# Performance work log

Measured on AMD Instinct MI355X. Metric: run time of the kernel, lower is better.

Reference implementation:

```python
import jax, jax.numpy as jnp
import numpy as np
import math

B, T, C = 4, 2048, 1024
N_HEADS = 16
D_HEAD = C // N_HEADS


def _rope_tables(d_head, max_seq_len):
    half = d_head // 2
    theta = 1.0 / (10000.0 ** (jnp.arange(half, dtype=jnp.float32) / half))
    pos = jnp.arange(max_seq_len, dtype=jnp.float32)
    freqs = jnp.outer(pos, theta)  # [S, half]
    cos = jnp.concatenate([jnp.cos(freqs), jnp.cos(freqs)], axis=-1)  # [S, d_head]
    sin = jnp.concatenate([jnp.sin(freqs), jnp.sin(freqs)], axis=-1)
    return cos, sin


def _rotate_half(x):
    d = x.shape[-1] // 2
    return jnp.concatenate([-x[..., d:], x[..., :d]], axis=-1)


def _apply_rope(x, cos, sin):
    # x: [B, H, T, d_head]; cos/sin: [T, d_head] broadcast over B,H
    return x * cos[None, None] + _rotate_half(x) * sin[None, None]


def setup_inputs() -> dict:
    key = jax.random.key(0)
    k1, k2, k3 = jax.random.split(key, 3)
    x = jax.random.normal(k1, (B, T, C), dtype=jnp.float32)
    W_qkv = jax.random.normal(k2, (C, 3 * C), dtype=jnp.float32) * (1.0 / math.sqrt(C))
    W_proj = jax.random.normal(k3, (C, C), dtype=jnp.float32) * (1.0 / math.sqrt(C))
    return {"x": x, "W_qkv": W_qkv, "W_proj": W_proj}


def reference(x, W_qkv, W_proj):
    b, t, c = x.shape
    qkv = x @ W_qkv  # [B, T, 3C]
    q, k, v = jnp.split(qkv, 3, axis=-1)

    def reshape(z):
        return z.reshape(b, t, N_HEADS, D_HEAD).transpose(0, 2, 1, 3)  # [B,H,T,dh]

    q, k, v = reshape(q), reshape(k), reshape(v)

    cos, sin = _rope_tables(D_HEAD, t)
    q = _apply_rope(q, cos, sin)
    k = _apply_rope(k, cos, sin)

    scale = 1.0 / math.sqrt(D_HEAD)
    att = jnp.einsum('bhqd,bhkd->bhqk', q, k) * scale  # [B,H,T,T]
    causal = jnp.tril(jnp.ones((t, t), dtype=bool))
    att = jnp.where(causal[None, None], att, -jnp.inf)
    att = jax.nn.softmax(att, axis=-1)
    out = jnp.einsum('bhqk,bhkd->bhqd', att, v)  # [B,H,T,dh]
    out = out.transpose(0, 2, 1, 3).reshape(b, t, c)
    return out @ W_proj
```

## Files before the change

kernel.cpp:

```cpp
#include <hip/hip_runtime.h>
#include <stdint.h>

#define Bz 4
#define Tz 2048
#define Cz 1024
#define NHz 16
#define DHz 64
#define Mz (Bz*Tz)

typedef unsigned short u16;
typedef __attribute__((ext_vector_type(8))) short short8;
typedef __attribute__((ext_vector_type(8))) unsigned short ushort8v;
typedef __attribute__((ext_vector_type(4))) unsigned short u16x4;
typedef __attribute__((ext_vector_type(4))) float f32x4;
typedef __attribute__((ext_vector_type(2))) unsigned int uint2v;

__device__ __forceinline__ float bf2f(u16 u){
  union { unsigned int i; float f; } v; v.i = ((unsigned int)u) << 16; return v.f;
}
__device__ __forceinline__ u16 f2bf(float f){
  union { float f; unsigned int i; } v; v.f = f;
  unsigned int r = v.i + 0x7FFFu + ((v.i >> 16) & 1u);
  return (u16)(r >> 16);
}


__global__ void k_cast_bf16(const float* __restrict__ in, u16* __restrict__ out, int n4){
  int i = blockIdx.x*256 + threadIdx.x;
  if (i >= n4) return;
  float4 v = ((const float4*)in)[i];
  u16x4 o;
  o[0] = f2bf(v.x); o[1] = f2bf(v.y); o[2] = f2bf(v.z); o[3] = f2bf(v.w);
  *(u16x4*)(out + (size_t)i*4) = o;
}

__global__ void k_transpose_cast(const float* __restrict__ W, u16* __restrict__ Wt, int K, int N){
  __shared__ float tile[32][33];
  int n0 = blockIdx.x*32, k0 = blockIdx.y*32;
  int tx = threadIdx.x, ty = threadIdx.y;
  #pragma unroll
  for (int i = 0; i < 32; i += 8)
    tile[ty+i][tx] = W[(size_t)(k0+ty+i)*N + n0 + tx];
  __syncthreads();
  #pragma unroll
  for (int i = 0; i < 32; i += 8)
    Wt[(size_t)(n0+ty+i)*K + k0 + tx] = f2bf(tile[tx][ty+i]);
}

__global__ void k_rope_tables(float* __restrict__ cosT, float* __restrict__ sinT){
  int idx = blockIdx.x*256 + threadIdx.x;
  int t = idx >> 5, i = idx & 31;
  float theta = exp2f(-(float)i * (13.287712379549449f / 32.0f));
  float ang = (float)t * theta;
  cosT[idx] = cosf(ang);
  sinT[idx] = sinf(ang);
}

#define GLDS(src, dstE) __builtin_amdgcn_global_load_lds( \
    (const __attribute__((address_space(1))) unsigned int*)(src), \
    (__attribute__((address_space(3))) unsigned int*)((u16*)lds + (dstE)), 16, 0, 0)

template<int Nn, int Kk, bool ROPE>
__global__ __launch_bounds__(256, 4) void k_gemmdb(const u16* __restrict__ A, const u16* __restrict__ Bt,
                        void* __restrict__ Cout, u16* __restrict__ vTout,
                        const float* __restrict__ cosT, const float* __restrict__ sinT){
  __shared__ u16 lds[2][16384];
  constexpr int NT = Kk/64;
  const int bm = blockIdx.x, bn = blockIdx.y;
  const int tid = threadIdx.x, lane = tid & 63, w = tid >> 6;
  const int wm = (w >> 1)*64, wn = (w & 1)*64;
  const int g = lane >> 4, r = lane & 15;

  const int srow8 = lane >> 3;
  const int sslot = (lane & 7) ^ srow8;
  const u16* asrc = A  + (size_t)(bm*128 + w*32 + srow8)*Kk + sslot*8;
  const u16* bsrc = Bt + (size_t)(bn*128 + w*32 + srow8)*Kk + sslot*8;
  const int dA = w*2048 + lane*8;
  const int dB = 8192 + w*2048 + lane*8;

  int a_off[4][2], b_off[4][2];
  #pragma unroll
  for (int i = 0; i < 4; ++i)
    #pragma unroll
    for (int kc = 0; kc < 2; ++kc){
      int row = wm + i*16 + r;
      a_off[i][kc] = (row*128 + kc*64 + g*16) ^ ((r & 7) << 4);
      int rowb = wn + i*16 + r;
      b_off[i][kc] = 16384 + ((rowb*128 + kc*64 + g*16) ^ ((r & 7) << 4));
    }

  f32x4 acc[4][4] = {};

#define STG(t, bi) do{ \
    const size_t ko_ = (size_t)(t)*64; \
    const int be_ = (bi)*16384; \
    GLDS(asrc + ko_,                 be_ + dA);        \
    GLDS(asrc + ko_ +  8*(size_t)Kk, be_ + dA + 512);  \
    GLDS(asrc + ko_ + 16*(size_t)Kk, be_ + dA + 1024); \
    GLDS(asrc + ko_ + 24*(size_t)Kk, be_ + dA + 1536); \
    GLDS(bsrc + ko_,                 be_ + dB);        \
    GLDS(bsrc + ko_ +  8*(size_t)Kk, be_ + dB + 512);  \
    GLDS(bsrc + ko_ + 16*(size_t)Kk, be_ + dB + 1024); \
    GLDS(bsrc + ko_ + 24*(size_t)Kk, be_ + dB + 1536); \
  }while(0)

  STG(0, 0);
  asm volatile("s_waitcnt vmcnt(0)" ::: "memory");
  __builtin_amdgcn_s_barrier();

  int buf = 0;
  #pragma unroll 1
  for (int t = 0; t < NT; ++t){
    if (t + 1 < NT) STG(t+1, buf^1);
    const char* Lb = (const char*)lds + buf*32768;
    short8 af[4][2], bf[4][2];
    #pragma unroll
    for (int i = 0; i < 4; ++i)
      #pragma unroll
      for (int kc = 0; kc < 2; ++kc){
        af[i][kc] = *(const short8*)(Lb + a_off[i][kc]);
        bf[i][kc] = *(const short8*)(Lb + b_off[i][kc]);
      }
    __builtin_amdgcn_s_setprio(1);
    #pragma unroll
    for (int i = 0; i < 4; ++i)
      #pragma unroll
      for (int j = 0; j < 4; ++j){
        acc[i][j] = __builtin_amdgcn_mfma_f32_16x16x32_bf16(af[i][0], bf[j][0], acc[i][j], 0,0,0);
        acc[i][j] = __builtin_amdgcn_mfma_f32_16x16x32_bf16(af[i][1], bf[j][1], acc[i][j], 0,0,0);
      }
    __builtin_amdgcn_s_setprio(0);
    if (t + 1 < NT){
      asm volatile("s_waitcnt vmcnt(0)" ::: "memory");
      __builtin_amdgcn_s_barrier();
      buf ^= 1;
    }
  }
#undef STG

  const int nbase = bn*128 + wn;
  if (ROPE && nbase >= 2048){
    const int b = bm >> 4;
    const int h = (nbase >> 6) & 15;
    #pragma unroll
    for (int ri = 0; ri < 4; ++ri){
      const int m0 = bm*128 + wm + ri*16 + 4*g;
      const int t0 = m0 & (Tz-1);
      #pragma unroll
      for (int cj = 0; cj < 4; ++cj){
        const int d = cj*16 + r;
        u16x4 o;
        #pragma unroll
        for (int jj = 0; jj < 4; ++jj) o[jj] = f2bf(acc[ri][cj][jj]);
        *(u16x4*)(vTout + ((size_t)((b*16 + h)*64 + d))*2048 + t0) = o;
      }
    }
  } else if (ROPE){
    const float qs = (nbase < 1024) ? 0.18033688011112042f : 1.0f;
    #pragma unroll
    for (int ri = 0; ri < 4; ++ri)
      #pragma unroll
      for (int jj = 0; jj < 4; ++jj){
        const int m = bm*128 + wm + ri*16 + 4*g + jj;
        const int t = m & (Tz-1);
        #pragma unroll
        for (int cj = 0; cj < 2; ++cj){
          const int ch = cj*16 + r;
          float cv = cosT[t*32 + ch];
          float sv = sinT[t*32 + ch];
          float lo = acc[ri][cj][jj], hi = acc[ri][cj+2][jj];
          ((u16*)Cout)[(size_t)m*Nn + nbase + ch]      = f2bf((lo*cv - hi*sv)*qs);
          ((u16*)Cout)[(size_t)m*Nn + nbase + ch + 32] = f2bf((hi*cv + lo*sv)*qs);
        }
      }
  } else {
    #pragma unroll
    for (int ri = 0; ri < 4; ++ri)
      #pragma unroll
      for (int cj = 0; cj < 4; ++cj)
        #pragma unroll
        for (int jj = 0; jj < 4; ++jj){
          const size_t m = bm*128 + wm + ri*16 + 4*g + jj;
          const size_t n = (size_t)nbase + cj*16 + r;
          ((float*)Cout)[m*Nn + n] = acc[ri][cj][jj];
        }
  }
}

__global__ __launch_bounds__(256) void k_attn3(const u16* __restrict__ qkv,
                                               const u16* __restrict__ vT,
                                               u16* __restrict__ att){
  __shared__ u16 K_lds[2*4096];
  __shared__ u16 V_lds[2*4096];
  __shared__ u16 P_lds[4*32*72];

  const int bh = blockIdx.x;
  const int b = bh >> 4, h = bh & 15;
  const int tid = threadIdx.x;
  const int w = tid >> 6;
  const int lane = tid & 63;
  const int g = lane >> 4;
  const int ql = lane & 15;
  u16* Pw = P_lds + w*32*72;

  const int srow  = lane >> 3;
  const int sslot = (lane & 7) ^ srow;
  const u16* ksrc = qkv + ((size_t)(b*Tz + 16*w + srow))*3072 + 1024 + h*64 + sslot*8;
  const u16* vsrc = vT  + ((size_t)bh*64 + 16*w + srow)*2048 + sslot*8;
  u16* kdst = K_lds + w*1024 + lane*8;
  u16* vdst = V_lds + w*1024 + lane*8;

  int fofs[4][2];
  #pragma unroll
  for (int t = 0; t < 4; ++t){
    int row = 16*t + ql;
    fofs[t][0] = (row*128 + 16*g)      ^ ((row & 7) << 4);
    fofs[t][1] = (row*128 + 64 + 16*g) ^ ((row & 7) << 4);
  }

#define STG_KV(kt, bi) do{ \
    const u16* ks_ = ksrc + (size_t)(kt)*64*3072; \
    const u16* vs_ = vsrc + (kt)*64; \
    u16* kd_ = kdst + (bi)*4096; \
    u16* vd_ = vdst + (bi)*4096; \
    __builtin_amdgcn_global_load_lds((const __attribute__((address_space(1))) unsigned int*)(ks_), \
        (__attribute__((address_space(3))) unsigned int*)(kd_), 16, 0, 0); \
    __builtin_amdgcn_global_load_lds((const __attribute__((address_space(1))) unsigned int*)(ks_ + 8*3072), \
        (__attribute__((address_space(3))) unsigned int*)(kd_ + 512), 16, 0, 0); \
    __builtin_amdgcn_global_load_lds((const __attribute__((address_space(1))) unsigned int*)(vs_), \
        (__attribute__((address_space(3))) unsigned int*)(vd_), 16, 0, 0); \
    __builtin_amdgcn_global_load_lds((const __attribute__((address_space(1))) unsigned int*)(vs_ + 8*2048), \
        (__attribute__((address_space(3))) unsigned int*)(vd_ + 512), 16, 0, 0); \
  }while(0)

  #pragma unroll 1
  for (int half = 0; half < 2; ++half){
    const int qt = (half == 0) ? blockIdx.y : (15 - blockIdx.y);
    const int qr0w = qt*128 + w*32;
    const int nt = 2*qt + 2;

    const u16* qsrcA = qkv + (size_t)(b*Tz + qr0w + ql)*3072 + h*64;
    const u16* qsrcB = qsrcA + 16*3072;
    short8 qfA0 = *(const short8*)(qsrcA + g*8);
    short8 qfA1 = *(const short8*)(qsrcA + 32 + g*8);
    short8 qfB0 = *(const short8*)(qsrcB + g*8);
    short8 qfB1 = *(const short8*)(qsrcB + 32 + g*8);

    f32x4 accA[4] = {{0,0,0,0},{0,0,0,0},{0,0,0,0},{0,0,0,0}};
    f32x4 accB[4] = {{0,0,0,0},{0,0,0,0},{0,0,0,0},{0,0,0,0}};
    float lrA = 0.0f, lrB = 0.0f;

    STG_KV(0, 0);
    __syncthreads();

    #pragma unroll 2
    for (int kt = 0; kt < nt; ++kt){
      const int buf = kt & 1;
      if (kt + 1 < nt) STG_KV(kt+1, buf^1);
      const char* Kb = (const char*)(K_lds + buf*4096);
      const char* Vb = (const char*)(V_lds + buf*4096);
      const int kv0 = kt*64;

      f32x4 stA[4], stB[4];
      __builtin_amdgcn_s_setprio(1);
      #pragma unroll
      for (int t = 0; t < 4; ++t){
        short8 kf0 = *(const short8*)(Kb + fofs[t][0]);
        short8 kf1 = *(const short8*)(Kb + fofs[t][1]);
        f32x4 zA = {0,0,0,0};
        zA = __builtin_amdgcn_mfma_f32_16x16x32_bf16(kf0, qfA0, zA, 0, 0, 0);
        zA = __builtin_amdgcn_mfma_f32_16x16x32_bf16(kf1, qfA1, zA, 0, 0, 0);
        stA[t] = zA;
        f32x4 zB = {0,0,0,0};
        zB = __builtin_amdgcn_mfma_f32_16x16x32_bf16(kf0, qfB0, zB, 0, 0, 0);
        zB = __builtin_amdgcn_mfma_f32_16x16x32_bf16(kf1, qfB1, zB, 0, 0, 0);
        stB[t] = zB;
      }
      __builtin_amdgcn_s_setprio(0);

      if (kv0 + 63 > qr0w){
        const int qg = qr0w + ql;
        #pragma unroll
        for (int t = 0; t < 4; ++t)
          #pragma unroll
          for (int j = 0; j < 4; ++j)
            if (kv0 + 16*t + 4*g + j > qg) stA[t][j] = -1e30f;
      }
      if (kv0 + 63 > qr0w + 16){
        const int qg = qr0w + 16 + ql;
        #pragma unroll
        for (int t = 0; t < 4; ++t)
          #pragma unroll
          for (int j = 0; j < 4; ++j)
            if (kv0 + 16*t + 4*g + j > qg) stB[t][j] = -1e30f;
      }

      #pragma unroll
      for (int t = 0; t < 4; ++t){
        float a0, a1, a2, a3, b0, b1, b2, b3;
        asm("v_exp_f32 %0, %1" : "=v"(a0) : "v"(stA[t][0]));
        asm("v_exp_f32 %0, %1" : "=v"(a1) : "v"(stA[t][1]));
        asm("v_exp_f32 %0, %1" : "=v"(a2) : "v"(stA[t][2]));
        asm("v_exp_f32 %0, %1" : "=v"(a3) : "v"(stA[t][3]));
        asm("v_exp_f32 %0, %1" : "=v"(b0) : "v"(stB[t][0]));
        asm("v_exp_f32 %0, %1" : "=v"(b1) : "v"(stB[t][1]));
        asm("v_exp_f32 %0, %1" : "=v"(b2) : "v"(stB[t][2]));
        asm("v_exp_f32 %0, %1" : "=v"(b3) : "v"(stB[t][3]));
        lrA += (a0+a1)+(a2+a3);
        lrB += (b0+b1)+(b2+b3);
        unsigned int wa0, wa1, wb0, wb1;
        asm("v_cvt_pk_bf16_f32 %0, %1, %2" : "=v"(wa0) : "v"(a0), "v"(a1));
        asm("v_cvt_pk_bf16_f32 %0, %1, %2" : "=v"(wa1) : "v"(a2), "v"(a3));
        asm("v_cvt_pk_bf16_f32 %0, %1, %2" : "=v"(wb0) : "v"(b0), "v"(b1));
        asm("v_cvt_pk_bf16_f32 %0, %1, %2" : "=v"(wb1) : "v"(b2), "v"(b3));
        uint2v pva; pva[0] = wa0; pva[1] = wa1;
        uint2v pvb; pvb[0] = wb0; pvb[1] = wb1;
        *(uint2v*)((char*)Pw + ql*144 + (16*t + 4*g)*2) = pva;
        *(uint2v*)((char*)Pw + (16 + ql)*144 + (16*t + 4*g)*2) = pvb;
      }

      short8 pfA0 = *(const short8*)((char*)Pw + ql*144 + 16*g);
      short8 pfA1 = *(const short8*)((char*)Pw + ql*144 + 64 + 16*g);
      short8 pfB0 = *(const short8*)((char*)Pw + (16 + ql)*144 + 16*g);
      short8 pfB1 = *(const short8*)((char*)Pw + (16 + ql)*144 + 64 + 16*g);

      __builtin_amdgcn_s_setprio(1);
      #pragma unroll
      for (int dt = 0; dt < 4; ++dt){
        short8 vf0 = *(const short8*)(Vb + fofs[dt][0]);
        short8 vf1 = *(const short8*)(Vb + fofs[dt][1]);
        accA[dt] = __builtin_amdgcn_mfma_f32_16x16x32_bf16(pfA0, vf0, accA[dt], 0, 0, 0);
        accA[dt] = __builtin_amdgcn_mfma_f32_16x16x32_bf16(pfA1, vf1, accA[dt], 0, 0, 0);
        accB[dt] = __builtin_amdgcn_mfma_f32_16x16x32_bf16(pfB0, vf0, accB[dt], 0, 0, 0);
        accB[dt] = __builtin_amdgcn_mfma_f32_16x16x32_bf16(pfB1, vf1, accB[dt], 0, 0, 0);
      }
      __builtin_amdgcn_s_setprio(0);
      __syncthreads();
    }

    lrA += __shfl_xor(lrA, 16); lrA += __shfl_xor(lrA, 32);
    lrB += __shfl_xor(lrB, 16); lrB += __shfl_xor(lrB, 32);
    float liA = 1.0f / lrA;
    float liB = 1.0f / lrB;
    float lA0 = __shfl(liA, 4*g+0), lA1 = __shfl(liA, 4*g+1);
    float lA2 = __shfl(liA, 4*g+2), lA3 = __shfl(liA, 4*g+3);
    float lB0 = __shfl(liB, 4*g+0), lB1 = __shfl(liB, 4*g+1);
    float lB2 = __shfl(liB, 4*g+2), lB3 = __shfl(liB, 4*g+3);
    #pragma unroll
    for (int dt = 0; dt < 4; ++dt){
      float ljA[4] = {lA0, lA1, lA2, lA3};
      float ljB[4] = {lB0, lB1, lB2, lB3};
      #pragma unroll
      for (int j = 0; j < 4; ++j){
        att[(size_t)(b*Tz + qr0w + 4*g + j)*Cz + h*64 + dt*16 + ql]      = f2bf(accA[dt][j]*ljA[j]);
        att[(size_t)(b*Tz + qr0w + 16 + 4*g + j)*Cz + h*64 + dt*16 + ql] = f2bf(accB[dt][j]*ljB[j]);
      }
    }
  }
#undef STG_KV
}


extern "C" void kernel_launch(void* const* d_in, const int* in_sizes, int n_in,
                              void* d_out, int out_size, void* d_ws, size_t ws_size,
                              hipStream_t stream){
  const float* x     = (const float*)d_in[0];
  const float* Wqkv  = (const float*)d_in[1];
  const float* Wproj = (const float*)d_in[2];
  float* out = (float*)d_out;
  char* ws = (char*)d_ws;

  u16*  xb   = (u16*)(ws);
  u16*  wqt  = (u16*)(ws + 16777216);
  u16*  wpt  = (u16*)(ws + 23068672);
  u16*  qkv  = (u16*)(ws + 25165824);
  u16*  vTr  = (u16*)(ws + 75497472);
  float* cosT = (float*)(ws + 92274688);
  float* sinT = (float*)(ws + 92536832);

  k_cast_bf16<<<Mz*Cz/4/256, 256, 0, stream>>>(x, xb, Mz*Cz/4);
  k_transpose_cast<<<dim3(3072/32, 1024/32), dim3(32,8), 0, stream>>>(Wqkv, wqt, 1024, 3072);
  k_transpose_cast<<<dim3(1024/32, 1024/32), dim3(32,8), 0, stream>>>(Wproj, wpt, 1024, 1024);
  k_rope_tables<<<Tz*32/256, 256, 0, stream>>>(cosT, sinT);

  k_gemmdb<3072, 1024, true><<<dim3(Mz/128, 3072/128), 256, 0, stream>>>(
      xb, wqt, qkv, vTr, cosT, sinT);
  k_attn3<<<dim3(Bz*NHz, 8), 256, 0, stream>>>(qkv, vTr, xb);
  k_gemmdb<1024, 1024, false><<<dim3(Mz/128, 1024/128), 256, 0, stream>>>(
      xb, wpt, out, nullptr, nullptr, nullptr);
}
```

Baseline: 172.7 us.

## Widen attention blocks to 256 query rows and fuse prep kernels

The attention kernel now uses 512 threads (8 waves), so each staged K/V tile in LDS is shared by 256 query rows instead of 128. It drops the paired light/heavy query-tile loop and instead orders blocks heaviest-first, with dynamic shared memory sized for the larger per-wave P buffers. Separately, the bf16 cast, the two weight transposes and the RoPE table kernels are merged into one launch to cut launch overhead. The trade-offs are uneven per-block work under the causal mask, higher LDS use per block that limits occupancy, and a per-call hipFuncSetAttribute on the host.

After: 226.2 us. 31.0% more time.

```diff
diff --git a/kernel.cpp b/kernel.cpp
--- a/kernel.cpp
+++ b/kernel.cpp
@@ -24,36 +24,40 @@
   return (u16)(r >> 16);
 }
 
-
-__global__ void k_cast_bf16(const float* __restrict__ in, u16* __restrict__ out, int n4){
-  int i = blockIdx.x*256 + threadIdx.x;
-  if (i >= n4) return;
-  float4 v = ((const float4*)in)[i];
-  u16x4 o;
-  o[0] = f2bf(v.x); o[1] = f2bf(v.y); o[2] = f2bf(v.z); o[3] = f2bf(v.w);
-  *(u16x4*)(out + (size_t)i*4) = o;
-}
-
-__global__ void k_transpose_cast(const float* __restrict__ W, u16* __restrict__ Wt, int K, int N){
+__global__ void k_prep(const float* __restrict__ x,     u16* __restrict__ xb,
+                       const float* __restrict__ Wqkv,  u16* __restrict__ wqt,
+                       const float* __restrict__ Wproj, u16* __restrict__ wpt,
+                       float* __restrict__ cosT, float* __restrict__ sinT){
   __shared__ float tile[32][33];
-  int n0 = blockIdx.x*32, k0 = blockIdx.y*32;
-  int tx = threadIdx.x, ty = threadIdx.y;
-  #pragma unroll
-  for (int i = 0; i < 32; i += 8)
-    tile[ty+i][tx] = W[(size_t)(k0+ty+i)*N + n0 + tx];
-  __syncthreads();
-  #pragma unroll
-  for (int i = 0; i < 32; i += 8)
-    Wt[(size_t)(n0+ty+i)*K + k0 + tx] = f2bf(tile[tx][ty+i]);
-}
-
-__global__ void k_rope_tables(float* __restrict__ cosT, float* __restrict__ sinT){
-  int idx = blockIdx.x*256 + threadIdx.x;
-  int t = idx >> 5, i = idx & 31;
-  float theta = exp2f(-(float)i * (13.287712379549449f / 32.0f));
-  float ang = (float)t * theta;
-  cosT[idx] = cosf(ang);
-  sinT[idx] = sinf(ang);
+  const int blk = blockIdx.x;
+  const int tid = threadIdx.x;
+  if (blk < 8192){
+    int i = blk*256 + tid;
+    float4 v = ((const float4*)x)[i];
+    u16x4 o;
+    o[0] = f2bf(v.x); o[1] = f2bf(v.y); o[2] = f2bf(v.z); o[3] = f2bf(v.w);
+    *(u16x4*)(xb + (size_t)i*4) = o;
+  } else if (blk < 12288){
+    const float* W; u16* Wt; int K, N, bx, by;
+    if (blk < 11264){ int b2 = blk - 8192;  W = Wqkv;  Wt = wqt; K = 1024; N = 3072; bx = b2 % 96; by = b2 / 96; }
+    else            { int b2 = blk - 11264; W = Wproj; Wt = wpt; K = 1024; N = 1024; bx = b2 % 32; by = b2 / 32; }
+    const int n0 = bx*32, k0 = by*32;
+    const int tx = tid & 31, ty = tid >> 5;
+    #pragma unroll
+    for (int i = 0; i < 32; i += 8)
+      tile[ty+i][tx] = W[(size_t)(k0+ty+i)*N + n0 + tx];
+    __syncthreads();
+    #pragma unroll
+    for (int i = 0; i < 32; i += 8)
+      Wt[(size_t)(n0+ty+i)*K + k0 + tx] = f2bf(tile[tx][ty+i]);
+  } else {
+    int idx = (blk - 12288)*256 + tid;
+    int t = idx >> 5, i = idx & 31;
+    float theta = exp2f(-(float)i * (13.287712379549449f / 32.0f));
+    float ang = (float)t * theta;
+    cosT[idx] = cosf(ang);
+    sinT[idx] = sinf(ang);
+  }
 }
 
 #define GLDS(src, dstE) __builtin_amdgcn_global_load_lds( \
@@ -187,28 +191,30 @@
   }
 }
 
-__global__ __launch_bounds__(256) void k_attn3(const u16* __restrict__ qkv,
-                                               const u16* __restrict__ vT,
-                                               u16* __restrict__ att){
-  __shared__ u16 K_lds[2*4096];
-  __shared__ u16 V_lds[2*4096];
-  __shared__ u16 P_lds[4*32*72];
+__global__ __launch_bounds__(512, 4) void k_attn3(const u16* __restrict__ qkv,
+                                                  const u16* __restrict__ vT,
+                                                  u16* __restrict__ att){
+  extern __shared__ u16 smem[];
+  u16* K_lds = smem;
+  u16* V_lds = smem + 8192;
+  u16* P_lds = smem + 16384;
 
   const int bh = blockIdx.x;
   const int b = bh >> 4, h = bh & 15;
+  const int qt2 = 7 - blockIdx.y;
   const int tid = threadIdx.x;
   const int w = tid >> 6;
   const int lane = tid & 63;
   const int g = lane >> 4;
   const int ql = lane & 15;
-  u16* Pw = P_lds + w*32*72;
+  u16* Pw = P_lds + w*2304;
 
   const int srow  = lane >> 3;
   const int sslot = (lane & 7) ^ srow;
-  const u16* ksrc = qkv + ((size_t)(b*Tz + 16*w + srow))*3072 + 1024 + h*64 + sslot*8;
-  const u16* vsrc = vT  + ((size_t)bh*64 + 16*w + srow)*2048 + sslot*8;
-  u16* kdst = K_lds + w*1024 + lane*8;
-  u16* vdst = V_lds + w*1024 + lane*8;
+  const u16* ksrc = qkv + ((size_t)(b*Tz + 8*w + srow))*3072 + 1024 + h*64 + sslot*8;
+  const u16* vsrc = vT  + ((size_t)bh*64 + 8*w + srow)*2048 + sslot*8;
+  u16* kdst = K_lds + w*512 + lane*8;
+  u16* vdst = V_lds + w*512 + lane*8;
 
   int fofs[4][2];
   #pragma unroll
@@ -218,146 +224,136 @@
     fofs[t][1] = (row*128 + 64 + 16*g) ^ ((row & 7) << 4);
   }
 
-#define STG_KV(kt, bi) do{ \
-    const u16* ks_ = ksrc + (size_t)(kt)*64*3072; \
-    const u16* vs_ = vsrc + (kt)*64; \
-    u16* kd_ = kdst + (bi)*4096; \
-    u16* vd_ = vdst + (bi)*4096; \
-    __builtin_amdgcn_global_load_lds((const __attribute__((address_space(1))) unsigned int*)(ks_), \
-        (__attribute__((address_space(3))) unsigned int*)(kd_), 16, 0, 0); \
-    __builtin_amdgcn_global_load_lds((const __attribute__((address_space(1))) unsigned int*)(ks_ + 8*3072), \
-        (__attribute__((address_space(3))) unsigned int*)(kd_ + 512), 16, 0, 0); \
-    __builtin_amdgcn_global_load_lds((const __attribute__((address_space(1))) unsigned int*)(vs_), \
-        (__attribute__((address_space(3))) unsigned int*)(vd_), 16, 0, 0); \
-    __builtin_amdgcn_global_load_lds((const __attribute__((address_space(1))) unsigned int*)(vs_ + 8*2048), \
-        (__attribute__((address_space(3))) unsigned int*)(vd_ + 512), 16, 0, 0); \
+#define STG_KV(kt_, bi_) do{ \
+    __builtin_amdgcn_global_load_lds( \
+      (const __attribute__((address_space(1))) unsigned int*)(ksrc + (size_t)(kt_)*64*3072), \
+      (__attribute__((address_space(3))) unsigned int*)(kdst + (bi_)*4096), 16, 0, 0); \
+    __builtin_amdgcn_global_load_lds( \
+      (const __attribute__((address_space(1))) unsigned int*)(vsrc + (kt_)*64), \
+      (__attribute__((address_space(3))) unsigned int*)(vdst + (bi_)*4096), 16, 0, 0); \
   }while(0)
 
-  #pragma unroll 1
-  for (int half = 0; half < 2; ++half){
-    const int qt = (half == 0) ? blockIdx.y : (15 - blockIdx.y);
-    const int qr0w = qt*128 + w*32;
-    const int nt = 2*qt + 2;
-
-    const u16* qsrcA = qkv + (size_t)(b*Tz + qr0w + ql)*3072 + h*64;
-    const u16* qsrcB = qsrcA + 16*3072;
-    short8 qfA0 = *(const short8*)(qsrcA + g*8);
-    short8 qfA1 = *(const short8*)(qsrcA + 32 + g*8);
-    short8 qfB0 = *(const short8*)(qsrcB + g*8);
-    short8 qfB1 = *(const short8*)(qsrcB + 32 + g*8);
-
-    f32x4 accA[4] = {{0,0,0,0},{0,0,0,0},{0,0,0,0},{0,0,0,0}};
-    f32x4 accB[4] = {{0,0,0,0},{0,0,0,0},{0,0,0,0},{0,0,0,0}};
-    float lrA = 0.0f, lrB = 0.0f;
-
-    STG_KV(0, 0);
+  const int qr0w = qt2*256 + w*32;
+  const int nt = (qt2 + 1)*4;
+
+  const u16* qsrcA = qkv + (size_t)(b*Tz + qr0w + ql)*3072 + h*64;
+  const u16* qsrcB = qsrcA + 16*3072;
+  short8 qfA0 = *(const short8*)(qsrcA + g*8);
+  short8 qfA1 = *(const short8*)(qsrcA + 32 + g*8);
+  short8 qfB0 = *(const short8*)(qsrcB + g*8);
+  short8 qfB1 = *(const short8*)(qsrcB + 32 + g*8);
+
+  f32x4 accA[4] = {{0,0,0,0},{0,0,0,0},{0,0,0,0},{0,0,0,0}};
+  f32x4 accB[4] = {{0,0,0,0},{0,0,0,0},{0,0,0,0},{0,0,0,0}};
+  float lrA = 0.0f, lrB = 0.0f;
+
+  STG_KV(0, 0);
+  __syncthreads();
+
+  #pragma unroll 2
+  for (int kt = 0; kt < nt; ++kt){
+    const int buf = kt & 1;
+    if (kt + 1 < nt) STG_KV(kt+1, buf^1);
+    const char* Kb = (const char*)(K_lds + buf*4096);
+    const char* Vb = (const char*)(V_lds + buf*4096);
+    const int kv0 = kt*64;
+
+    f32x4 stA[4], stB[4];
+    __builtin_amdgcn_s_setprio(1);
+    #pragma unroll
+    for (int t = 0; t < 4; ++t){
+      short8 kf0 = *(const short8*)(Kb + fofs[t][0]);
+      short8 kf1 = *(const short8*)(Kb + fofs[t][1]);
+      f32x4 zA = {0,0,0,0};
+      zA = __builtin_amdgcn_mfma_f32_16x16x32_bf16(kf0, qfA0, zA, 0, 0, 0);
+      zA = __builtin_amdgcn_mfma_f32_16x16x32_bf16(kf1, qfA1, zA, 0, 0, 0);
+      stA[t] = zA;
+      f32x4 zB = {0,0,0,0};
+      zB = __builtin_amdgcn_mfma_f32_16x16x32_bf16(kf0, qfB0, zB, 0, 0, 0);
+      zB = __builtin_amdgcn_mfma_f32_16x16x32_bf16(kf1, qfB1, zB, 0, 0, 0);
+      stB[t] = zB;
+    }
+    __builtin_amdgcn_s_setprio(0);
+
+    if (kv0 + 63 > qr0w){
+      const int qg = qr0w + ql;
+      #pragma unroll
+      for (int t = 0; t < 4; ++t)
+        #pragma unroll
+        for (int j = 0; j < 4; ++j)
+          if (kv0 + 16*t + 4*g + j > qg) stA[t][j] = -1e30f;
+    }
+    if (kv0 + 63 > qr0w + 16){
+      const int qg = qr0w + 16 + ql;
+      #pragma unroll
+      for (int t = 0; t < 4; ++t)
+        #pragma unroll
+        for (int j = 0; j < 4; ++j)
+          if (kv0 + 16*t + 4*g + j > qg) stB[t][j] = -1e30f;
+    }
+
+    #pragma unroll
+    for (int t = 0; t < 4; ++t){
+      float a0, a1, a2, a3, b0, b1, b2, b3;
+      asm("v_exp_f32 %0, %1" : "=v"(a0) : "v"(stA[t][0]));
+      asm("v_exp_f32 %0, %1" : "=v"(a1) : "v"(stA[t][1]));
+      asm("v_exp_f32 %0, %1" : "=v"(a2) : "v"(stA[t][2]));
+      asm("v_exp_f32 %0, %1" : "=v"(a3) : "v"(stA[t][3]));
+      asm("v_exp_f32 %0, %1" : "=v"(b0) : "v"(stB[t][0]));
+      asm("v_exp_f32 %0, %1" : "=v"(b1) : "v"(stB[t][1]));
+      asm("v_exp_f32 %0, %1" : "=v"(b2) : "v"(stB[t][2]));
+      asm("v_exp_f32 %0, %1" : "=v"(b3) : "v"(stB[t][3]));
+      lrA += (a0+a1)+(a2+a3);
+      lrB += (b0+b1)+(b2+b3);
+      unsigned int wa0, wa1, wb0, wb1;
+      asm("v_cvt_pk_bf16_f32 %0, %1, %2" : "=v"(wa0) : "v"(a0), "v"(a1));
+      asm("v_cvt_pk_bf16_f32 %0, %1, %2" : "=v"(wa1) : "v"(a2), "v"(a3));
+      asm("v_cvt_pk_bf16_f32 %0, %1, %2" : "=v"(wb0) : "v"(b0), "v"(b1));
+      asm("v_cvt_pk_bf16_f32 %0, %1, %2" : "=v"(wb1) : "v"(b2), "v"(b3));
+      uint2v pva; pva[0] = wa0; pva[1] = wa1;
+      uint2v pvb; pvb[0] = wb0; pvb[1] = wb1;
+      *(uint2v*)((char*)Pw + ql*144 + (16*t + 4*g)*2) = pva;
+      *(uint2v*)((char*)Pw + (16 + ql)*144 + (16*t + 4*g)*2) = pvb;
+    }
+
+    short8 pfA0 = *(const short8*)((char*)Pw + ql*144 + 16*g);
+    short8 pfA1 = *(const short8*)((char*)Pw + ql*144 + 64 + 16*g);
+    short8 pfB0 = *(const short8*)((char*)Pw + (16 + ql)*144 + 16*g);
+    short8 pfB1 = *(const short8*)((char*)Pw + (16 + ql)*144 + 64 + 16*g);
+
+    __builtin_amdgcn_s_setprio(1);
+    #pragma unroll
+    for (int dt = 0; dt < 4; ++dt){
+      short8 vf0 = *(const short8*)(Vb + fofs[dt][0]);
+      short8 vf1 = *(const short8*)(Vb + fofs[dt][1]);
+      accA[dt] = __builtin_amdgcn_mfma_f32_16x16x32_bf16(pfA0, vf0, accA[dt], 0, 0, 0);
+      accA[dt] = __builtin_amdgcn_mfma_f32_16x16x32_bf16(pfA1, vf1, accA[dt], 0, 0, 0);
+      accB[dt] = __builtin_amdgcn_mfma_f32_16x16x32_bf16(pfB0, vf0, accB[dt], 0, 0, 0);
+      accB[dt] = __builtin_amdgcn_mfma_f32_16x16x32_bf16(pfB1, vf1, accB[dt], 0, 0, 0);
+    }
+    __builtin_amdgcn_s_setprio(0);
     __syncthreads();
-
-    #pragma unroll 2
-    for (int kt = 0; kt < nt; ++kt){
-      const int buf = kt & 1;
-      if (kt + 1 < nt) STG_KV(kt+1, buf^1);
-      const char* Kb = (const char*)(K_lds + buf*4096);
-      const char* Vb = (const char*)(V_lds + buf*4096);
-      const int kv0 = kt*64;
-
-      f32x4 stA[4], stB[4];
-      __builtin_amdgcn_s_setprio(1);
-      #pragma unroll
-      for (int t = 0; t < 4; ++t){
-        short8 kf0 = *(const short8*)(Kb + fofs[t][0]);
-        short8 kf1 = *(const short8*)(Kb + fofs[t][1]);
-        f32x4 zA = {0,0,0,0};
-        zA = __builtin_amdgcn_mfma_f32_16x16x32_bf16(kf0, qfA0, zA, 0, 0, 0);
-        zA = __builtin_amdgcn_mfma_f32_16x16x32_bf16(kf1, qfA1, zA, 0, 0, 0);
-        stA[t] = zA;
-        f32x4 zB = {0,0,0,0};
-        zB = __builtin_amdgcn_mfma_f32_16x16x32_bf16(kf0, qfB0, zB, 0, 0, 0);
-        zB = __builtin_amdgcn_mfma_f32_16x16x32_bf16(kf1, qfB1, zB, 0, 0, 0);
-        stB[t] = zB;
-      }
-      __builtin_amdgcn_s_setprio(0);
-
-      if (kv0 + 63 > qr0w){
-        const int qg = qr0w + ql;
-        #pragma unroll
-        for (int t = 0; t < 4; ++t)
-          #pragma unroll
-          for (int j = 0; j < 4; ++j)
-            if (kv0 + 16*t + 4*g + j > qg) stA[t][j] = -1e30f;
-      }
-      if (kv0 + 63 > qr0w + 16){
-        const int qg = qr0w + 16 + ql;
-        #pragma unroll
-        for (int t = 0; t < 4; ++t)
-          #pragma unroll
-          for (int j = 0; j < 4; ++j)
-            if (kv0 + 16*t + 4*g + j > qg) stB[t][j] = -1e30f;
-      }
-
-      #pragma unroll
-      for (int t = 0; t < 4; ++t){
-        float a0, a1, a2, a3, b0, b1, b2, b3;
-        asm("v_exp_f32 %0, %1" : "=v"(a0) : "v"(stA[t][0]));
-        asm("v_exp_f32 %0, %1" : "=v"(a1) : "v"(stA[t][1]));
-        asm("v_exp_f32 %0, %1" : "=v"(a2) : "v"(stA[t][2]));
-        asm("v_exp_f32 %0, %1" : "=v"(a3) : "v"(stA[t][3]));
-        asm("v_exp_f32 %0, %1" : "=v"(b0) : "v"(stB[t][0]));
-        asm("v_exp_f32 %0, %1" : "=v"(b1) : "v"(stB[t][1]));
-        asm("v_exp_f32 %0, %1" : "=v"(b2) : "v"(stB[t][2]));
-        asm("v_exp_f32 %0, %1" : "=v"(b3) : "v"(stB[t][3]));
-        lrA += (a0+a1)+(a2+a3);
-        lrB += (b0+b1)+(b2+b3);
-        unsigned int wa0, wa1, wb0, wb1;
-        asm("v_cvt_pk_bf16_f32 %0, %1, %2" : "=v"(wa0) : "v"(a0), "v"(a1));
-        asm("v_cvt_pk_bf16_f32 %0, %1, %2" : "=v"(wa1) : "v"(a2), "v"(a3));
-        asm("v_cvt_pk_bf16_f32 %0, %1, %2" : "=v"(wb0) : "v"(b0), "v"(b1));
-        asm("v_cvt_pk_bf16_f32 %0, %1, %2" : "=v"(wb1) : "v"(b2), "v"(b3));
-        uint2v pva; pva[0] = wa0; pva[1] = wa1;
-        uint2v pvb; pvb[0] = wb0; pvb[1] = wb1;
-        *(uint2v*)((char*)Pw + ql*144 + (16*t + 4*g)*2) = pva;
-        *(uint2v*)((char*)Pw + (16 + ql)*144 + (16*t + 4*g)*2) = pvb;
-      }
-
-      short8 pfA0 = *(const short8*)((char*)Pw + ql*144 + 16*g);
-      short8 pfA1 = *(const short8*)((char*)Pw + ql*144 + 64 + 16*g);
-      short8 pfB0 = *(const short8*)((char*)Pw + (16 + ql)*144 + 16*g);
-      short8 pfB1 = *(const short8*)((char*)Pw + (16 + ql)*144 + 64 + 16*g);
-
-      __builtin_amdgcn_s_setprio(1);
-      #pragma unroll
-      for (int dt = 0; dt < 4; ++dt){
-        short8 vf0 = *(const short8*)(Vb + fofs[dt][0]);
-        short8 vf1 = *(const short8*)(Vb + fofs[dt][1]);
-        accA[dt] = __builtin_amdgcn_mfma_f32_16x16x32_bf16(pfA0, vf0, accA[dt], 0, 0, 0);
-        accA[dt] = __builtin_amdgcn_mfma_f32_16x16x32_bf16(pfA1, vf1, accA[dt], 0, 0, 0);
-        accB[dt] = __builtin_amdgcn_mfma_f32_16x16x32_bf16(pfB0, vf0, accB[dt], 0, 0, 0);
-        accB[dt] = __builtin_amdgcn_mfma_f32_16x16x32_bf16(pfB1, vf1, accB[dt], 0, 0, 0);
-      }
-      __builtin_amdgcn_s_setprio(0);
-      __syncthreads();
-    }
-
-    lrA += __shfl_xor(lrA, 16); lrA += __shfl_xor(lrA, 32);
-    lrB += __shfl_xor(lrB, 16); lrB += __shfl_xor(lrB, 32);
-    float liA = 1.0f / lrA;
-    float liB = 1.0f / lrB;
-    float lA0 = __shfl(liA, 4*g+0), lA1 = __shfl(liA, 4*g+1);
-    float lA2 = __shfl(liA, 4*g+2), lA3 = __shfl(liA, 4*g+3);
-    float lB0 = __shfl(liB, 4*g+0), lB1 = __shfl(liB, 4*g+1);
-    float lB2 = __shfl(liB, 4*g+2), lB3 = __shfl(liB, 4*g+3);
-    #pragma unroll
-    for (int dt = 0; dt < 4; ++dt){
-      float ljA[4] = {lA0, lA1, lA2, lA3};
-      float ljB[4] = {lB0, lB1, lB2, lB3};
-      #pragma unroll
-      for (int j = 0; j < 4; ++j){
-        att[(size_t)(b*Tz + qr0w + 4*g + j)*Cz + h*64 + dt*16 + ql]      = f2bf(accA[dt][j]*ljA[j]);
-        att[(size_t)(b*Tz + qr0w + 16 + 4*g + j)*Cz + h*64 + dt*16 + ql] = f2bf(accB[dt][j]*ljB[j]);
-      }
-    }
   }
 #undef STG_KV
+
+  lrA += __shfl_xor(lrA, 16); lrA += __shfl_xor(lrA, 32);
+  lrB += __shfl_xor(lrB, 16); lrB += __shfl_xor(lrB, 32);
+  float liA = 1.0f / lrA;
+  float liB = 1.0f / lrB;
+  float lA0 = __shfl(liA, 4*g+0), lA1 = __shfl(liA, 4*g+1);
+  float lA2 = __shfl(liA, 4*g+2), lA3 = __shfl(liA, 4*g+3);
+  float lB0 = __shfl(liB, 4*g+0), lB1 = __shfl(liB, 4*g+1);
+  float lB2 = __shfl(liB, 4*g+2), lB3 = __shfl(liB, 4*g+3);
+  #pragma unroll
+  for (int dt = 0; dt < 4; ++dt){
+    float ljA[4] = {lA0, lA1, lA2, lA3};
+    float ljB[4] = {lB0, lB1, lB2, lB3};
+    #pragma unroll
+    for (int j = 0; j < 4; ++j){
+      att[(size_t)(b*Tz + qr0w + 4*g + j)*Cz + h*64 + dt*16 + ql]      = f2bf(accA[dt][j]*ljA[j]);
+      att[(size_t)(b*Tz + qr0w + 16 + 4*g + j)*Cz + h*64 + dt*16 + ql] = f2bf(accB[dt][j]*ljB[j]);
+    }
+  }
 }
 
 
@@ -378,14 +374,14 @@
   float* cosT = (float*)(ws + 92274688);
   float* sinT = (float*)(ws + 92536832);
 
-  k_cast_bf16<<<Mz*Cz/4/256, 256, 0, stream>>>(x, xb, Mz*Cz/4);
-  k_transpose_cast<<<dim3(3072/32, 1024/32), dim3(32,8), 0, stream>>>(Wqkv, wqt, 1024, 3072);
-  k_transpose_cast<<<dim3(1024/32, 1024/32), dim3(32,8), 0, stream>>>(Wproj, wpt, 1024, 1024);
-  k_rope_tables<<<Tz*32/256, 256, 0, stream>>>(cosT, sinT);
+  hipFuncSetAttribute(reinterpret_cast<const void*>(k_attn3),
+                      hipFuncAttributeMaxDynamicSharedMemorySize, 69632);
+
+  k_prep<<<12544, 256, 0, stream>>>(x, xb, Wqkv, wqt, Wproj, wpt, cosT, sinT);
 
   k_gemmdb<3072, 1024, true><<<dim3(Mz/128, 3072/128), 256, 0, stream>>>(
       xb, wqt, qkv, vTr, cosT, sinT);
-  k_attn3<<<dim3(Bz*NHz, 8), 256, 0, stream>>>(qkv, vTr, xb);
+  k_attn3<<<dim3(Bz*NHz, 8), 512, 69632, stream>>>(qkv, vTr, xb);
   k_gemmdb<1024, 1024, false><<<dim3(Mz/128, 1024/128), 256, 0, stream>>>(
       xb, wpt, out, nullptr, nullptr, nullptr);
 }
```
